# Performance work log

Hardware: AMD Instinct MI355X
Metric: run time of the kernel (lower is better)

The kernel has to match this reference:

```python
import jax, jax.numpy as jnp
import numpy as np

B, N, IN_DIM, HID, K = 8, 4096, 10, 64, 8
NORM = np.array([1.0/2950.0, 1.0/2950.0, 1.0/2950.0, 1.0/5.265625, 1.0/143.875,
                 1.0/589.0, 1.0/1.2050781, 1.0/211.0, 1.0, 1.0/7.0], dtype=np.float32)


def _lin(key, fan_in, fan_out):
    k1, k2 = jax.random.split(key)
    s = 1.0 / np.sqrt(fan_in)
    w = jax.random.uniform(k1, (fan_in, fan_out), jnp.float32, -s, s)
    b = jax.random.uniform(k2, (fan_out,), jnp.float32, -s, s)
    return w, b


def setup_inputs() -> dict:
    key = jax.random.key(0)
    ks = jax.random.split(key, 10)
    x = jax.random.normal(ks[0], (B, N, IN_DIM), jnp.float32)
    w_in1, b_in1 = _lin(ks[1], IN_DIM, HID // 2)
    w_in2, b_in2 = _lin(ks[2], HID // 2, HID)
    w_c1a, b_c1a = _lin(ks[3], 2 * HID, 3 * HID // 2)
    w_c1b, b_c1b = _lin(ks[4], 3 * HID // 2, HID)
    w_c2a, b_c2a = _lin(ks[5], 2 * HID, 3 * HID // 2)
    w_c2b, b_c2b = _lin(ks[6], 3 * HID // 2, HID)
    w_o1, b_o1 = _lin(ks[7], HID, HID)
    w_o2, b_o2 = _lin(ks[8], HID, HID // 2)
    w_o3, b_o3 = _lin(ks[9], HID // 2, 2)
    return dict(x=x, datanorm=jnp.asarray(NORM),
                w_in1=w_in1, b_in1=b_in1, w_in2=w_in2, b_in2=b_in2,
                w_c1a=w_c1a, b_c1a=b_c1a, w_c1b=w_c1b, b_c1b=b_c1b,
                w_c2a=w_c2a, b_c2a=b_c2a, w_c2b=w_c2b, b_c2b=b_c2b,
                w_o1=w_o1, b_o1=b_o1, w_o2=w_o2, b_o2=b_o2, w_o3=w_o3, b_o3=b_o3)


def _knn(x, k):
    # x: [B, n, H] -> [B, n, k] indices of k nearest neighbors (self excluded)
    x2 = jnp.sum(x * x, -1)
    d = x2[:, :, None] + x2[:, None, :] - 2.0 * jnp.einsum('bnh,bmh->bnm', x, x)
    n = x.shape[1]
    d = d + jnp.eye(n, dtype=x.dtype) * 1e9
    return jax.lax.top_k(-d, k)[1]


def _edge_conv(x, nbr, w1, b1, w2, b2):
    # EdgeConv with max aggregation over undirected kNN edges.
    # message(i <- j) = MLP([x_i, x_j - x_i]); edges symmetrized (j->i and i->j).
    b, n, k = nbr.shape
    dst0 = jnp.broadcast_to(jnp.arange(n)[None, :, None], (b, n, k)).reshape(b, n * k)
    src0 = nbr.reshape(b, n * k)
    src = jnp.concatenate([src0, dst0], 1)  # [b, 2nk]
    dst = jnp.concatenate([dst0, src0], 1)
    xd = jnp.take_along_axis(x, dst[..., None], 1)
    xs = jnp.take_along_axis(x, src[..., None], 1)
    m = jnp.concatenate([xd, xs - xd], -1)           # [b, 2nk, 2H]
    m = jax.nn.elu(m @ w1 + b1)
    m = jax.nn.elu(m @ w2 + b2)
    seg = lambda mm, dd: jax.ops.segment_max(mm, dd, num_segments=n)
    return jax.vmap(seg)(m, dst)                     # [b, n, H]


def reference(x, datanorm, w_in1, b_in1, w_in2, b_in2,
              w_c1a, b_c1a, w_c1b, b_c1b, w_c2a, b_c2a, w_c2b, b_c2b,
              w_o1, b_o1, w_o2, b_o2, w_o3, b_o3):
    h = x * datanorm
    h = jax.nn.elu(h @ w_in1 + b_in1)
    h = jax.nn.elu(h @ w_in2 + b_in2)
    nbr = _knn(jax.lax.stop_gradient(h), K)          # knn_graph is non-differentiable
    h = _edge_conv(h, nbr, w_c1a, b_c1a, w_c1b, b_c1b)
    # deterministic pairwise max-pool (stand-in for graclus+max_pool, halves node count)
    h = h.reshape(B, N // 2, 2, HID).max(2)
    nbr = _knn(jax.lax.stop_gradient(h), K)
    h = _edge_conv(h, nbr, w_c2a, b_c2a, w_c2b, b_c2b)
    # second graclus max_pool_x followed by global_max_pool == global max pool
    g = h.max(1)                                     # [B, HID]
    o = jax.nn.elu(g @ w_o1 + b_o1)
    o = jax.nn.elu(o @ w_o2 + b_o2)
    o = o @ w_o3 + b_o3                              # [B, 2]
    met = jax.nn.softplus(o[:, :1])
    metphi = jnp.pi * (2.0 * jax.nn.sigmoid(o[:, 1:2]) - 1.0)
    return jnp.concatenate([met, metphi], 1)
```

## Files before the change

kernel.cpp:

```cpp
#include <hip/hip_runtime.h>
#include <hip/hip_bf16.h>

#define BATCH 8
#define N1 4096
#define N2 2048
#define HID 64
#define KNN 8
#define INDIM 10

using u64 = unsigned long long;
using bf16 = __hip_bfloat16;
typedef __attribute__((ext_vector_type(8))) short short8;
typedef __attribute__((ext_vector_type(4))) float f32x4;

__device__ __align__(256) float    g_h1[BATCH * N1 * HID];
__device__ __align__(256) float    g_h2[BATCH * N2 * HID];
__device__ __align__(256) float    g_x2n[BATCH * N1];
__device__ __align__(256) float    g_x2n2[BATCH * N2];
__device__ __align__(256) int      g_nbr[BATCH * N1 * KNN];
__device__ __align__(256) float    g_uu[BATCH * N1 * 96];
__device__ __align__(256) float    g_vv[BATCH * N1 * 96];
__device__ __align__(256) unsigned g_ek1[BATCH * N1 * HID];
__device__ __align__(256) unsigned g_ek2[BATCH * N2 * HID];
__device__ __align__(256) short    g_f1[BATCH * N1 * HID];
__device__ __align__(256) short    g_f2[BATCH * N1 * HID];
__device__ __align__(256) short    g_f3[BATCH * N1 * HID];
__device__ __align__(256) float    g_uf[BATCH * N1 * 96];
__device__ __align__(256) float    g_vf[BATCH * N1 * 96];
__device__ __align__(256) short    g_wf1[2 * 4 * 3 * 64 * 8];
__device__ __align__(256) short    g_wf2[2 * 4 * 3 * 64 * 8];

__device__ __forceinline__ float eluf(float x) { return x > 0.f ? x : __expf(x) - 1.f; }
__device__ __forceinline__ unsigned encf(float f) {
  unsigned u = __float_as_uint(f);
  return u ^ ((unsigned)((int)u >> 31) | 0x80000000u);
}
__device__ __forceinline__ float decf(unsigned k) {
  unsigned u = (k & 0x80000000u) ? (k & 0x7FFFFFFFu) : ~k;
  return __uint_as_float(u);
}
#define ENC_NEG1 0x407FFFFFu
__device__ __forceinline__ unsigned enc_safe(float v) {
  if (!(v == v)) return ENC_NEG1;
  return encf(v);
}
__device__ __forceinline__ float dec_safe(unsigned k) {
  float v = decf(k);
  if (!(v == v)) return -1.0f;
  return fminf(fmaxf(v, -3.0e38f), 3.0e38f);
}
__device__ __forceinline__ unsigned umed3(unsigned a, unsigned b, unsigned c) {
  unsigned d;
  asm("v_med3_u32 %0, %1, %2, %3" : "=v"(d) : "v"(a), "v"(b), "v"(c));
  return d;
}
__device__ __forceinline__ void split3(float v, short& b1, short& b2, short& b3) {
  bf16 x1 = __float2bfloat16(v);
  float r1 = v - __bfloat162float(x1);
  bf16 x2 = __float2bfloat16(r1);
  float r2 = r1 - __bfloat162float(x2);
  bf16 x3 = __float2bfloat16(r2);
  b1 = *(short*)&x1; b2 = *(short*)&x2; b3 = *(short*)&x3;
}
__device__ __forceinline__ void split2(float v, short& b1, short& b2) {
  bf16 x1 = __float2bfloat16(v);
  float r1 = v - __bfloat162float(x1);
  bf16 x2 = __float2bfloat16(r1);
  b1 = *(short*)&x1; b2 = *(short*)&x2;
}
__device__ __forceinline__ void store_frags(int node, const short* s1,
                                            const short* s2, const short* s3) {
  size_t tb = ((size_t)(node >> 4)) * 1024 + (node & 15) * 8;
#pragma unroll
  for (int chunk = 0; chunk < 2; ++chunk) {
#pragma unroll
    for (int q = 0; q < 4; ++q) {
      size_t a = tb + chunk * 512 + q * 128;
      int k = chunk * 32 + q * 8;
      *(short8*)(g_f1 + a) = *(const short8*)(s1 + k);
      *(short8*)(g_f2 + a) = *(const short8*)(s2 + k);
      *(short8*)(g_f3 + a) = *(const short8*)(s3 + k);
    }
  }
}
__device__ __forceinline__ void tv_frag(float4 a0, float4 a1, float4 b0,
                                        float4 b1, short8& s1, short8& s2) {
  float v[8] = {a0.x + b0.x, a0.y + b0.y, a0.z + b0.z, a0.w + b0.w,
                a1.x + b1.x, a1.y + b1.y, a1.z + b1.z, a1.w + b1.w};
#pragma unroll
  for (int e = 0; e < 8; ++e) {
    float t = eluf(v[e]);
    short p1, p2;
    split2(t, p1, p2);
    s1[e] = p1; s2[e] = p2;
  }
}

__global__ __launch_bounds__(256) void prep_kernel(
    const float* __restrict__ x, const float* __restrict__ norm,
    const float* __restrict__ w1g, const float* __restrict__ b1g,
    const float* __restrict__ w2g, const float* __restrict__ b2g,
    const float* __restrict__ wc1b, const float* __restrict__ wc2b) {
  int bid = blockIdx.x;
  int t = threadIdx.x;
  if (bid < 128) {
    __shared__ float sw1[320], sb1[32], sw2[2048], sb2[64], snorm[INDIM];
    for (int q = t; q < 320; q += 256) sw1[q] = w1g[q];
    for (int q = t; q < 2048; q += 256) sw2[q] = w2g[q];
    if (t < 32) sb1[t] = b1g[t];
    if (t < 64) sb2[t] = b2g[t];
    if (t < INDIM) snorm[t] = norm[t];
    __syncthreads();
    int node = bid * 256 + t;
    float xv[INDIM];
#pragma unroll
    for (int d = 0; d < INDIM; ++d)
      xv[d] = x[(size_t)node * INDIM + d] * snorm[d];
    float t1[32];
#pragma unroll
    for (int c = 0; c < 32; ++c) {
      float acc = sb1[c];
#pragma unroll
      for (int d = 0; d < INDIM; ++d) acc += xv[d] * sw1[d * 32 + c];
      t1[c] = eluf(acc);
    }
    float* hr = g_h1 + (size_t)node * HID;
    float sq = 0.f;
    short s1l[HID], s2l[HID], s3l[HID];
#pragma unroll
    for (int c = 0; c < HID; ++c) {
      float acc = sb2[c];
#pragma unroll
      for (int d = 0; d < 32; ++d) acc += t1[d] * sw2[d * HID + c];
      float v = eluf(acc);
      hr[c] = v;
      sq += v * v;
      split3(v, s1l[c], s2l[c], s3l[c]);
    }
    store_frags(node, s1l, s2l, s3l);
    g_x2n[node] = sq;
  } else if (bid < 130) {
    int level = bid - 128;
    const float* w = level ? wc2b : wc1b;
    for (int idx = t; idx < 6144; idx += 256) {
      int no = idx / 1536;
      int rem = idx - no * 1536;
      int kc = rem / 512;
      int rem2 = rem - kc * 512;
      int lane = rem2 >> 3;
      int j = rem2 & 7;
      int k = kc * 32 + (lane >> 4) * 8 + j;
      int o = no * 16 + (lane & 15);
      short b1, b2;
      split2(w[k * 64 + o], b1, b2);
      g_wf1[level * 6144 + idx] = b1;
      g_wf2[level * 6144 + idx] = b2;
    }
  } else {
    int tt = (bid - 130) * 256 + t;
    uint4 z = make_uint4(ENC_NEG1, ENC_NEG1, ENC_NEG1, ENC_NEG1);
    const int n1 = BATCH * N1 * HID / 4;
    if (tt < n1) ((uint4*)g_ek1)[tt] = z;
    else ((uint4*)g_ek2)[tt - n1] = z;
  }
}

template <int LEVEL>
__device__ __forceinline__ void knn_body(unsigned* lm) {
  constexpr int n = LEVEL ? N2 : N1;
  constexpr int NT = n / 16;
  constexpr int HT = NT / 2;
  constexpr int NSET = LEVEL ? 1 : 2;
  constexpr int SS = NSET * 16;

  int b = blockIdx.x & 7;
  int rb = (blockIdx.x >> 3) * (2 * SS);
  int t = threadIdx.x;
  int wv = t >> 6, lane = t & 63;
  int s = wv >> 1, hf = wv & 1;
  int q = lane >> 4, c = lane & 15;
  const float* __restrict__ x2b = (LEVEL ? g_x2n2 : g_x2n) + (size_t)b * n;
  size_t abase = ((size_t)((b * n + rb + s * SS) >> 4)) * 1024 + lane * 8;
  short8 A1a[NSET], A1b[NSET], A2a[NSET], A2b[NSET], A3a[NSET], A3b[NSET];
#pragma unroll
  for (int e = 0; e < NSET; ++e) {
    size_t ab = abase + (size_t)e * 1024;
    A1a[e] = *(const short8*)(g_f1 + ab);
    A1b[e] = *(const short8*)(g_f1 + ab + 512);
    A2a[e] = *(const short8*)(g_f2 + ab);
    A2b[e] = *(const short8*)(g_f2 + ab + 512);
    A3a[e] = *(const short8*)(g_f3 + ab);
    A3b[e] = *(const short8*)(g_f3 + ab + 512);
  }
  unsigned best[NSET][4][KNN];
#pragma unroll
  for (int e = 0; e < NSET; ++e)
#pragma unroll
    for (int r = 0; r < 4; ++r)
#pragma unroll
      for (int p = 0; p < KNN; ++p) best[e][r][p] = 0xFFFFFFFFu;
  const int ct0 = hf * HT;
  const int selftile = (rb + s * SS) >> 4;
  const f32x4 zero = {0.f, 0.f, 0.f, 0.f};
  size_t bb = ((size_t)(b * n) >> 4) * 1024 + (size_t)ct0 * 1024 + lane * 8;

  short8 Pa[6], Pb[6];
  float xa, xb;
  auto LOADB = [&](short8* P, size_t addr) {
    P[0] = *(const short8*)(g_f1 + addr);
    P[1] = *(const short8*)(g_f1 + addr + 512);
    P[2] = *(const short8*)(g_f2 + addr);
    P[3] = *(const short8*)(g_f2 + addr + 512);
    P[4] = *(const short8*)(g_f3 + addr);
    P[5] = *(const short8*)(g_f3 + addr + 512);
  };
  auto COMPUTE = [&](const short8* P, float x2c, int ct) {
#pragma unroll
    for (int e = 0; e < NSET; ++e) {
      f32x4 acc0 = __builtin_amdgcn_mfma_f32_16x16x32_bf16(A1a[e], P[0], zero, 0, 0, 0);
      f32x4 acc1 = __builtin_amdgcn_mfma_f32_16x16x32_bf16(A1b[e], P[1], zero, 0, 0, 0);
      acc0 = __builtin_amdgcn_mfma_f32_16x16x32_bf16(A1a[e], P[2], acc0, 0, 0, 0);
      acc1 = __builtin_amdgcn_mfma_f32_16x16x32_bf16(A1b[e], P[3], acc1, 0, 0, 0);
      acc0 = __builtin_amdgcn_mfma_f32_16x16x32_bf16(A2a[e], P[0], acc0, 0, 0, 0);
      acc1 = __builtin_amdgcn_mfma_f32_16x16x32_bf16(A2b[e], P[1], acc1, 0, 0, 0);
      acc0 = __builtin_amdgcn_mfma_f32_16x16x32_bf16(A1a[e], P[4], acc0, 0, 0, 0);
      acc1 = __builtin_amdgcn_mfma_f32_16x16x32_bf16(A1b[e], P[5], acc1, 0, 0, 0);
      acc0 = __builtin_amdgcn_mfma_f32_16x16x32_bf16(A2a[e], P[2], acc0, 0, 0, 0);
      acc1 = __builtin_amdgcn_mfma_f32_16x16x32_bf16(A2b[e], P[3], acc1, 0, 0, 0);
      acc0 = __builtin_amdgcn_mfma_f32_16x16x32_bf16(A3a[e], P[0], acc0, 0, 0, 0);
      acc1 = __builtin_amdgcn_mfma_f32_16x16x32_bf16(A3b[e], P[1], acc1, 0, 0, 0);
      unsigned ck[4];
#pragma unroll
      for (int r = 0; r < 4; ++r) {
        float sm2 = acc0[r] + acc1[r];
        float dd = __builtin_fmaf(-2.f, sm2, x2c);
        ck[r] = (encf(dd) & 0xFFFFFF00u) | (unsigned)ct;
      }
      if (ct == selftile + e) {
#pragma unroll
        for (int r = 0; r < 4; ++r)
          if (c == q * 4 + r) ck[r] = 0xFFFFFFFFu;
      }
#pragma unroll
      for (int r = 0; r < 4; ++r) {
        unsigned x = ck[r];
#pragma unroll
        for (int p = KNN - 1; p >= 1; --p)
          best[e][r][p] = umed3(best[e][r][p - 1], best[e][r][p], x);
        best[e][r][0] = min(best[e][r][0], x);
      }
    }
  };

  LOADB(Pa, bb);
  xa = x2b[ct0 * 16 + c];
  for (int tt = 0; tt < HT; tt += 2) {
    int ct = ct0 + tt;
    LOADB(Pb, bb + 1024);
    xb = x2b[(ct + 1) * 16 + c];
    COMPUTE(Pa, xa, ct);
    size_t nb2 = (tt + 2 < HT) ? bb + 2048 : bb;
    int ctn2 = (tt + 2 < HT) ? ct + 2 : ct;
    LOADB(Pa, nb2);
    xa = x2b[ctn2 * 16 + c];
    COMPUTE(Pb, xb, ct + 1);
    bb += 2048;
  }
#pragma unroll
  for (int pass = 0; pass < NSET; ++pass) {
#pragma unroll
    for (int r = 0; r < 4; ++r) {
      int lrow = s * 16 + q * 4 + r;
      unsigned* dst = lm + lrow * 289 + (hf * 16 + c) * 9;
#pragma unroll
      for (int p = 0; p < KNN; ++p) dst[p] = best[pass][r][p];
    }
    __syncthreads();
    {
      int arow = t >> 3, am = t & 7;
      unsigned* base = lm + arow * 289;
      const unsigned* l0 = base + (am * 4) * 9;
      u64 fin[KNN];
#pragma unroll
      for (int p = 0; p < KNN; ++p)
        fin[p] = (((u64)l0[p]) << 4) | (unsigned)((am * 4) & 15);
      for (int d = 1; d < 4; ++d) {
        const unsigned* ld = base + (am * 4 + d) * 9;
        unsigned cb = (unsigned)((am * 4 + d) & 15);
        for (int p = 0; p < KNN; ++p) {
          u64 ckk = (((u64)ld[p]) << 4) | cb;
          if (ckk >= fin[KNN - 1]) break;
#pragma unroll
          for (int p2 = 0; p2 < KNN; ++p2) {
            u64 ob = fin[p2];
            bool ex = ob < ckk;
            fin[p2] = ex ? ob : ckk;
            ckk = ex ? ckk : ob;
          }
        }
      }
      unsigned* dst = base + (am * 4) * 9;
#pragma unroll
      for (int p = 0; p < KNN; ++p) {
        dst[2 * p] = (unsigned)fin[p];
        dst[2 * p + 1] = (unsigned)(fin[p] >> 32);
      }
    }
    __syncthreads();
    if (t < 64) {
      int brow = t >> 1, bm = t & 1;
      unsigned* base = lm + brow * 289;
      u64 fin[KNN];
      {
        const unsigned* s0 = base + (bm * 4) * 36;
#pragma unroll
        for (int p = 0; p < KNN; ++p)
          fin[p] = (((u64)s0[2 * p + 1]) << 32) | s0[2 * p];
      }
      for (int d = 1; d < 4; ++d) {
        const unsigned* sd = base + (bm * 4 + d) * 36;
        for (int p = 0; p < KNN; ++p) {
          u64 ckk = (((u64)sd[2 * p + 1]) << 32) | sd[2 * p];
          if (ckk >= fin[KNN - 1]) break;
#pragma unroll
          for (int p2 = 0; p2 < KNN; ++p2) {
            u64 ob = fin[p2];
            bool ex = ob < ckk;
            fin[p2] = ex ? ob : ckk;
            ckk = ex ? ckk : ob;
          }
        }
      }
      unsigned* dst = base + (bm * 4) * 36;
#pragma unroll
      for (int p = 0; p < KNN; ++p) {
        dst[2 * p] = (unsigned)fin[p];
        dst[2 * p + 1] = (unsigned)(fin[p] >> 32);
      }
    }
    __syncthreads();
    if (t < 32) {
      unsigned* base = lm + t * 289;
      u64 fin[KNN];
#pragma unroll
      for (int p = 0; p < KNN; ++p)
        fin[p] = (((u64)base[2 * p + 1]) << 32) | base[2 * p];
      const unsigned* s1 = base + 144;
      for (int p = 0; p < KNN; ++p) {
        u64 ckk = (((u64)s1[2 * p + 1]) << 32) | s1[2 * p];
        if (ckk >= fin[KNN - 1]) break;
#pragma unroll
        for (int p2 = 0; p2 < KNN; ++p2) {
          u64 ob = fin[p2];
          bool ex = ob < ckk;
          fin[p2] = ex ? ob : ckk;
          ckk = ex ? ckk : ob;
        }
      }
      int row = rb + (t >> 4) * SS + pass * 16 + (t & 15);
      int* ob = g_nbr + ((size_t)b * n + row) * KNN;
#pragma unroll
      for (int p = 0; p < KNN; ++p) {
        int j = (int)((fin[p] >> 4) & 255u) * 16 + (int)(fin[p] & 15u);
        ob[p] = j & (n - 1);
      }
    }
    if (pass + 1 < NSET) __syncthreads();
  }
}

template <int LEVEL>
__device__ __forceinline__ void uv_body(float* sw1, float* sb1, int ub,
                                        const float* __restrict__ w1g,
                                        const float* __restrict__ b1g) {
  int t = threadIdx.x;
  for (int q = t; q < 128 * 96; q += 256) sw1[q] = w1g[q];
  if (t < 96) sb1[t] = b1g[t];
  __syncthreads();
  const int n = LEVEL ? N2 : N1;
  const float* h = LEVEL ? g_h2 : g_h1;
  int b = ub & 7;
  int nl = (ub >> 3) * 64 + (t & 63);
  int c0 = (t >> 6) * 24;
  size_t node = (size_t)b * n + nl;
  const float4* h4 = (const float4*)(h + node * HID);
  float ua[24], va[24];
#pragma unroll
  for (int c = 0; c < 24; ++c) { ua[c] = 0.f; va[c] = 0.f; }
  float4 vv = h4[0];
  for (int qd = 0; qd < 16; ++qd) {
    float4 cur = vv;
    if (qd < 15) vv = h4[qd + 1];
    float el[4] = {cur.x, cur.y, cur.z, cur.w};
#pragma unroll
    for (int j = 0; j < 4; ++j) {
      int d = qd * 4 + j;
      float hd = el[j];
      const float* wt = sw1 + d * 96 + c0;
      const float* wb = sw1 + (HID + d) * 96 + c0;
#pragma unroll
      for (int c = 0; c < 24; ++c) {
        ua[c] += hd * wt[c];
        va[c] += hd * wb[c];
      }
    }
  }
  float* ur = g_uu + node * 96 + c0;
  float* vr = g_vv + node * 96 + c0;
#pragma unroll
  for (int c = 0; c < 24; ++c) {
    float uval = ua[c] - va[c] + sb1[c0 + c];
    float vval = va[c];
    ur[c] = uval;
    vr[c] = vval;
    int kk = c0 + c;
    size_t fa = (node >> 4) * 1536 + (size_t)((kk >> 5) * 512 +
                ((kk >> 3) & 3) * 128 + (nl & 15) * 8 + (kk & 7));
    g_uf[fa] = uval;
    g_vf[fa] = vval;
  }
}

template <int LEVEL>
__global__ __launch_bounds__(256, 2) void knuv_kernel(
    const float* __restrict__ w1g, const float* __restrict__ b1g) {
  constexpr int KB = LEVEL ? (8 * (N2 / 32)) : (8 * (N1 / 64));
  __shared__ __align__(16) unsigned char smem[49536];
  if ((int)blockIdx.x < KB) {
    knn_body<LEVEL>((unsigned*)smem);
  } else {
    uv_body<LEVEL>((float*)smem, (float*)(smem + 49152),
                   (int)blockIdx.x - KB, w1g, b1g);
  }
}

template <int LEVEL>
__global__ __launch_bounds__(256, 1) void edge_kernel(
    const float* __restrict__ b2g) {
  constexpr int n = LEVEL ? N2 : N1;
  unsigned* ekey = LEVEL ? g_ek2 : g_ek1;
  int b = blockIdx.x & 7;
  int t = threadIdx.x;
  int wv = t >> 6, lane = t & 63;
  int q = lane >> 4, c = lane & 15;
  int base16 = (blockIdx.x >> 3) * 64 + wv * 16;
  int node_c = base16 + c;
  const int* nbb = g_nbr + (size_t)b * n * KNN;
  const float* ub = g_uu + (size_t)b * n * 96;
  const float* vb = g_vv + (size_t)b * n * 96;
  size_t ftile = ((size_t)(b * n + base16) >> 4) * 1536;
  unsigned* eb = ekey + (size_t)b * n * HID;
  short8 W1f[4][3], W2f[4][3];
#pragma unroll
  for (int no = 0; no < 4; ++no)
#pragma unroll
    for (int kc = 0; kc < 3; ++kc) {
      int off = LEVEL * 6144 + ((no * 3 + kc) * 64 + lane) * 8;
      W1f[no][kc] = *(const short8*)(g_wf1 + off);
      W2f[no][kc] = *(const short8*)(g_wf2 + off);
    }
  float biasv[4];
#pragma unroll
  for (int no = 0; no < 4; ++no) biasv[no] = b2g[no * 16 + c];
  float macc[16];
#pragma unroll
  for (int e = 0; e < 16; ++e) macc[e] = -1.0f;
  for (int slot = 0; slot < KNN; ++slot) {
    int jn = nbb[(size_t)node_c * KNN + slot] & (n - 1);
    short8 t1[3], t2[3], r1[3], r2[3];
#pragma unroll
    for (int kc = 0; kc < 3; ++kc) {
      size_t fo = ftile + kc * 512 + lane * 8;
      float4 su0 = *(const float4*)(g_uf + fo);
      float4 su1 = *(const float4*)(g_uf + fo + 4);
      float4 sv0 = *(const float4*)(g_vf + fo);
      float4 sv1 = *(const float4*)(g_vf + fo + 4);
      size_t go = (size_t)jn * 96 + kc * 32 + q * 8;
      float4 gv0 = *(const float4*)(vb + go);
      float4 gv1 = *(const float4*)(vb + go + 4);
      float4 gu0 = *(const float4*)(ub + go);
      float4 gu1 = *(const float4*)(ub + go + 4);
      tv_frag(su0, su1, gv0, gv1, t1[kc], t2[kc]);
      tv_frag(gu0, gu1, sv0, sv1, r1[kc], r2[kc]);
    }
    f32x4 aF[4], aR[4];
#pragma unroll
    for (int no = 0; no < 4; ++no) {
      aF[no] = (f32x4){0.f, 0.f, 0.f, 0.f};
      aR[no] = (f32x4){0.f, 0.f, 0.f, 0.f};
    }
#pragma unroll
    for (int no = 0; no < 4; ++no)
#pragma unroll
      for (int kc = 0; kc < 3; ++kc) {
        aF[no] = __builtin_amdgcn_mfma_f32_16x16x32_bf16(t1[kc], W1f[no][kc], aF[no], 0, 0, 0);
        aF[no] = __builtin_amdgcn_mfma_f32_16x16x32_bf16(t2[kc], W1f[no][kc], aF[no], 0, 0, 0);
        aF[no] = __builtin_amdgcn_mfma_f32_16x16x32_bf16(t1[kc], W2f[no][kc], aF[no], 0, 0, 0);
        aR[no] = __builtin_amdgcn_mfma_f32_16x16x32_bf16(r1[kc], W1f[no][kc], aR[no], 0, 0, 0);
        aR[no] = __builtin_amdgcn_mfma_f32_16x16x32_bf16(r2[kc], W1f[no][kc], aR[no], 0, 0, 0);
        aR[no] = __builtin_amdgcn_mfma_f32_16x16x32_bf16(r1[kc], W2f[no][kc], aR[no], 0, 0, 0);
      }
#pragma unroll
    for (int r = 0; r < 4; ++r) {
      int jr = nbb[(size_t)(base16 + q * 4 + r) * KNN + slot] & (n - 1);
#pragma unroll
      for (int no = 0; no < 4; ++no) {
        float mv = eluf(aR[no][r] + biasv[no]);
        atomicMax(&eb[(size_t)jr * HID + no * 16 + c], enc_safe(mv));
      }
    }
#pragma unroll
    for (int no = 0; no < 4; ++no)
#pragma unroll
      for (int r = 0; r < 4; ++r)
        macc[no * 4 + r] = fmaxf(macc[no * 4 + r], eluf(aF[no][r] + biasv[no]));
  }
#pragma unroll
  for (int r = 0; r < 4; ++r) {
    size_t ib = (size_t)(base16 + q * 4 + r) * HID;
#pragma unroll
    for (int no = 0; no < 4; ++no)
      atomicMax(&eb[ib + no * 16 + c], enc_safe(macc[no * 4 + r]));
  }
}

__global__ __launch_bounds__(256) void pool_kernel() {
  int node = blockIdx.x * 256 + threadIdx.x;
  int b = node >> 11;
  int m = node & (N2 - 1);
  const unsigned* e = g_ek1 + ((size_t)b * N1 + 2 * m) * HID;
  float* hr = g_h2 + (size_t)node * HID;
  float sq = 0.f;
  short s1l[HID], s2l[HID], s3l[HID];
#pragma unroll
  for (int d = 0; d < HID; ++d) {
    float mx = fmaxf(dec_safe(e[d]), dec_safe(e[HID + d]));
    hr[d] = mx;
    sq += mx * mx;
    split3(mx, s1l[d], s2l[d], s3l[d]);
  }
  store_frags(node, s1l, s2l, s3l);
  g_x2n2[node] = sq;
}

__global__ __launch_bounds__(256) void final_kernel(
    const float* __restrict__ wo1, const float* __restrict__ bo1,
    const float* __restrict__ wo2, const float* __restrict__ bo2,
    const float* __restrict__ wo3, const float* __restrict__ bo3,
    float* __restrict__ out) {
  __shared__ unsigned red[4][HID];
  __shared__ float g[HID];
  __shared__ float o1s[HID];
  __shared__ float o2s[32];
  int b = blockIdx.x;
  int t = threadIdx.x;
  int grp = t >> 6, d = t & 63;
  const unsigned* e = g_ek2 + (size_t)b * N2 * HID;
  unsigned mk = 0u;
  for (int m = grp; m < N2; m += 4) {
    unsigned qv = e[(size_t)m * HID + d];
    mk = qv > mk ? qv : mk;
  }
  red[grp][d] = mk;
  __syncthreads();
  if (t < HID) {
    unsigned q1 = red[0][t] > red[1][t] ? red[0][t] : red[1][t];
    unsigned q2 = red[2][t] > red[3][t] ? red[2][t] : red[3][t];
    g[t] = dec_safe(q1 > q2 ? q1 : q2);
  }
  __syncthreads();
  if (t < HID) {
    float a1 = bo1[t];
    for (int dd = 0; dd < HID; ++dd) a1 += g[dd] * wo1[dd * HID + t];
    o1s[t] = eluf(a1);
  }
  __syncthreads();
  if (t < 32) {
    float a2 = bo2[t];
    for (int dd = 0; dd < HID; ++dd) a2 += o1s[dd] * wo2[dd * 32 + t];
    o2s[t] = eluf(a2);
  }
  __syncthreads();
  if (t == 0) {
    float acc0 = bo3[0];
    float acc1 = bo3[1];
    for (int dd = 0; dd < 32; ++dd) {
      acc0 += o2s[dd] * wo3[dd * 2 + 0];
      acc1 += o2s[dd] * wo3[dd * 2 + 1];
    }
    float met = fmaxf(acc0, 0.f) + log1pf(expf(-fabsf(acc0)));
    float phi = 3.14159265358979f * (2.f / (1.f + expf(-acc1)) - 1.f);
    out[b * 2 + 0] = met;
    out[b * 2 + 1] = phi;
  }
}

extern "C" void kernel_launch(void* const* d_in, const int* in_sizes, int n_in,
                              void* d_out, int out_size, void* d_ws,
                              size_t ws_size, hipStream_t stream) {
  const float* x     = (const float*)d_in[0];
  const float* dnorm = (const float*)d_in[1];
  const float* w_in1 = (const float*)d_in[2];
  const float* b_in1 = (const float*)d_in[3];
  const float* w_in2 = (const float*)d_in[4];
  const float* b_in2 = (const float*)d_in[5];
  const float* w_c1a = (const float*)d_in[6];
  const float* b_c1a = (const float*)d_in[7];
  const float* w_c1b = (const float*)d_in[8];
  const float* b_c1b = (const float*)d_in[9];
  const float* w_c2a = (const float*)d_in[10];
  const float* b_c2a = (const float*)d_in[11];
  const float* w_c2b = (const float*)d_in[12];
  const float* b_c2b = (const float*)d_in[13];
  const float* w_o1  = (const float*)d_in[14];
  const float* b_o1  = (const float*)d_in[15];
  const float* w_o2  = (const float*)d_in[16];
  const float* b_o2  = (const float*)d_in[17];
  const float* w_o3  = (const float*)d_in[18];
  const float* b_o3  = (const float*)d_in[19];

  prep_kernel<<<3202, 256, 0, stream>>>(x, dnorm, w_in1, b_in1, w_in2, b_in2,
                                        w_c1b, w_c2b);
  knuv_kernel<0><<<1024, 256, 0, stream>>>(w_c1a, b_c1a);
  edge_kernel<0><<<8 * (N1 / 64), 256, 0, stream>>>(b_c1b);
  pool_kernel<<<BATCH * N2 / 256, 256, 0, stream>>>();
  knuv_kernel<1><<<768, 256, 0, stream>>>(w_c2a, b_c2a);
  edge_kernel<1><<<8 * (N2 / 64), 256, 0, stream>>>(b_c2b);
  final_kernel<<<BATCH, 256, 0, stream>>>(w_o1, b_o1, w_o2, b_o2, w_o3, b_o3,
                                          (float*)d_out);
}
```

Measured before the change: 496.1 us.

## Fuse edge+pool and edge+final kernels using atomic completion counters

Merges the level-0 edge kernel with the pool kernel, and the level-1 edge kernel with the final head kernel. Each fused launch uses a global done counter that is reset in prep_kernel: edge blocks increment it, and the tail blocks spin until every edge block has finished. This removes two kernel launches and their gaps. It relies on the edge blocks being scheduled before or alongside the spinning blocks, which is a deadlock risk if the waiting blocks occupy CUs first. The edge body also loses its launch_bounds(256,1) occupancy hint, which may change register allocation.

```diff
diff --git a/kernel.cpp b/kernel.cpp
--- a/kernel.cpp
+++ b/kernel.cpp
@@ -29,6 +29,8 @@
 __device__ __align__(256) float    g_vf[BATCH * N1 * 96];
 __device__ __align__(256) short    g_wf1[2 * 4 * 3 * 64 * 8];
 __device__ __align__(256) short    g_wf2[2 * 4 * 3 * 64 * 8];
+__device__ unsigned g_done1;
+__device__ unsigned g_done2;
 
 __device__ __forceinline__ float eluf(float x) { return x > 0.f ? x : __expf(x) - 1.f; }
 __device__ __forceinline__ unsigned encf(float f) {
@@ -103,6 +105,7 @@
     const float* __restrict__ wc1b, const float* __restrict__ wc2b) {
   int bid = blockIdx.x;
   int t = threadIdx.x;
+  if (bid == 0 && t == 0) { g_done1 = 0u; g_done2 = 0u; }
   if (bid < 128) {
     __shared__ float sw1[320], sb1[32], sw2[2048], sb2[64], snorm[INDIM];
     for (int q = t; q < 320; q += 256) sw1[q] = w1g[q];
@@ -435,8 +438,7 @@
 }
 
 template <int LEVEL>
-__global__ __launch_bounds__(256, 1) void edge_kernel(
-    const float* __restrict__ b2g) {
+__device__ __forceinline__ void edge_body(const float* __restrict__ b2g) {
   constexpr int n = LEVEL ? N2 : N1;
   unsigned* ekey = LEVEL ? g_ek2 : g_ek1;
   int b = blockIdx.x & 7;
@@ -524,8 +526,8 @@
   }
 }
 
-__global__ __launch_bounds__(256) void pool_kernel() {
-  int node = blockIdx.x * 256 + threadIdx.x;
+__device__ __forceinline__ void pool_unit(int u) {
+  int node = u * 256 + threadIdx.x;
   int b = node >> 11;
   int m = node & (N2 - 1);
   const unsigned* e = g_ek1 + ((size_t)b * N1 + 2 * m) * HID;
@@ -543,16 +545,33 @@
   g_x2n2[node] = sq;
 }
 
-__global__ __launch_bounds__(256) void final_kernel(
-    const float* __restrict__ wo1, const float* __restrict__ bo1,
+__global__ __launch_bounds__(256) void edgepool_kernel(
+    const float* __restrict__ b2g) {
+  int bid = blockIdx.x;
+  if (bid < 512) {
+    edge_body<0>(b2g);
+    __syncthreads();
+    __threadfence();
+    if (threadIdx.x == 0) atomicAdd(&g_done1, 1u);
+  } else {
+    if (threadIdx.x == 0) {
+      while (atomicAdd(&g_done1, 0u) < 512u) __builtin_amdgcn_s_sleep(8);
+    }
+    __syncthreads();
+    __threadfence();
+    pool_unit(bid - 512);
+  }
+}
+
+__device__ __forceinline__ void final_body(
+    int b, const float* __restrict__ wo1, const float* __restrict__ bo1,
     const float* __restrict__ wo2, const float* __restrict__ bo2,
     const float* __restrict__ wo3, const float* __restrict__ bo3,
-    float* __restrict__ out) {
-  __shared__ unsigned red[4][HID];
-  __shared__ float g[HID];
-  __shared__ float o1s[HID];
-  __shared__ float o2s[32];
-  int b = blockIdx.x;
+    float* __restrict__ out, unsigned char* smem) {
+  unsigned* red = (unsigned*)smem;
+  float* g = (float*)(smem + 1024);
+  float* o1s = (float*)(smem + 1280);
+  float* o2s = (float*)(smem + 1536);
   int t = threadIdx.x;
   int grp = t >> 6, d = t & 63;
   const unsigned* e = g_ek2 + (size_t)b * N2 * HID;
@@ -561,11 +580,12 @@
     unsigned qv = e[(size_t)m * HID + d];
     mk = qv > mk ? qv : mk;
   }
-  red[grp][d] = mk;
+  red[grp * HID + d] = mk;
   __syncthreads();
   if (t < HID) {
-    unsigned q1 = red[0][t] > red[1][t] ? red[0][t] : red[1][t];
-    unsigned q2 = red[2][t] > red[3][t] ? red[2][t] : red[3][t];
+    unsigned q1 = red[t] > red[HID + t] ? red[t] : red[HID + t];
+    unsigned q2 = red[2 * HID + t] > red[3 * HID + t] ? red[2 * HID + t]
+                                                      : red[3 * HID + t];
     g[t] = dec_safe(q1 > q2 ? q1 : q2);
   }
   __syncthreads();
@@ -592,6 +612,29 @@
     float phi = 3.14159265358979f * (2.f / (1.f + expf(-acc1)) - 1.f);
     out[b * 2 + 0] = met;
     out[b * 2 + 1] = phi;
+  }
+}
+
+__global__ __launch_bounds__(256) void edgefinal_kernel(
+    const float* __restrict__ b2g,
+    const float* __restrict__ wo1, const float* __restrict__ bo1,
+    const float* __restrict__ wo2, const float* __restrict__ bo2,
+    const float* __restrict__ wo3, const float* __restrict__ bo3,
+    float* __restrict__ out) {
+  __shared__ __align__(16) unsigned char smem[1664];
+  int bid = blockIdx.x;
+  if (bid < 256) {
+    edge_body<1>(b2g);
+    __syncthreads();
+    __threadfence();
+    if (threadIdx.x == 0) atomicAdd(&g_done2, 1u);
+  } else {
+    if (threadIdx.x == 0) {
+      while (atomicAdd(&g_done2, 0u) < 256u) __builtin_amdgcn_s_sleep(8);
+    }
+    __syncthreads();
+    __threadfence();
+    final_body(bid - 256, wo1, bo1, wo2, bo2, wo3, bo3, out, smem);
   }
 }
 
@@ -622,10 +665,8 @@
   prep_kernel<<<3202, 256, 0, stream>>>(x, dnorm, w_in1, b_in1, w_in2, b_in2,
                                         w_c1b, w_c2b);
   knuv_kernel<0><<<1024, 256, 0, stream>>>(w_c1a, b_c1a);
-  edge_kernel<0><<<8 * (N1 / 64), 256, 0, stream>>>(b_c1b);
-  pool_kernel<<<BATCH * N2 / 256, 256, 0, stream>>>();
+  edgepool_kernel<<<576, 256, 0, stream>>>(b_c1b);
   knuv_kernel<1><<<768, 256, 0, stream>>>(w_c2a, b_c2a);
-  edge_kernel<1><<<8 * (N2 / 64), 256, 0, stream>>>(b_c2b);
-  final_kernel<<<BATCH, 256, 0, stream>>>(w_o1, b_o1, w_o2, b_o2, w_o3, b_o3,
-                                          (float*)d_out);
-}
+  edgefinal_kernel<<<264, 256, 0, stream>>>(b_c2b, w_o1, b_o1, w_o2, b_o2,
+                                            w_o3, b_o3, (float*)d_out);
+}
```

New measurement: 537.6 us. 8.4% more time.
